# Kernel tuning notes

Hardware: AMD Instinct MI355X
Metric: run time of the kernel (lower is better)

## Reference

```python
import jax, jax.numpy as jnp
import numpy as np

S, D, E = 8192, 128, 48  # seq_len, embedding_dim, num pos tags (experts)

def setup_inputs() -> dict:
    key = jax.random.key(0)
    ks = jax.random.split(key, 8)
    sc = 1.0 / np.sqrt(D)
    return {
        "embs": jax.random.normal(ks[0], (S, D), dtype=jnp.float32),
        "pos_ids": jax.random.randint(ks[1], (S,), 0, E),
        "W_exp": jax.random.normal(ks[2], (E, D, D), dtype=jnp.float32) * sc,
        "b_exp": jax.random.normal(ks[3], (E, D), dtype=jnp.float32) * sc,
        "W_ih": jax.random.normal(ks[4], (4 * D, D), dtype=jnp.float32) * sc,
        "W_hh": jax.random.normal(ks[5], (4 * D, D), dtype=jnp.float32) * sc,
        "b_ih": jax.random.normal(ks[6], (4 * D,), dtype=jnp.float32) * sc,
        "b_hh": jax.random.normal(ks[7], (4 * D,), dtype=jnp.float32) * sc,
    }

def reference(embs, pos_ids, W_exp, b_exp, W_ih, W_hh, b_ih, b_hh):
    d = embs.shape[1]
    # --- per-token expert Linear (pos-tag-routed) ---
    # gather expert weights per token: [S, D, D], then per-token GEMV
    Wg = W_exp[pos_ids]                      # [S, D, D]
    bg = b_exp[pos_ids]                      # [S, D]
    z = jnp.einsum('sij,sj->si', Wg, embs) + bg  # [S, D]
    # --- 1-layer LSTM (PyTorch gate order: i, f, g, o) ---
    x_gates = z @ W_ih.T + b_ih + b_hh       # [S, 4D], precompute input contribution
    def step(carry, xg):
        h, c = carry
        gates = xg + h @ W_hh.T              # [4D]
        i, f, g, o = jnp.split(gates, 4)
        i = jax.nn.sigmoid(i)
        f = jax.nn.sigmoid(f)
        g = jnp.tanh(g)
        o = jax.nn.sigmoid(o)
        c = f * c + i * g
        h = o * jnp.tanh(c)
        return (h, c), h
    h0 = jnp.zeros((d,), dtype=embs.dtype)
    c0 = jnp.zeros((d,), dtype=embs.dtype)
    _, hs = jax.lax.scan(step, (h0, c0), x_gates)  # hs: [S, D]
    # --- max-pool over time; batch dim of 1 as in the torch module ---
    out = jnp.max(hs, axis=0)[None, :]       # [1, D]
    return out
```

## Files before the change

kernel.cpp:

```cpp
#include <hip/hip_runtime.h>
#include <math.h>


#define SEQ   8192
#define DIM   128
#define NGATE 512
#define NEXP  48

typedef _Float16 v8h  __attribute__((ext_vector_type(8)));
typedef float    v4f  __attribute__((ext_vector_type(4)));

__device__ __forceinline__ float sigm_fast(float x) {
    return __fdividef(1.0f, 1.0f + __expf(-x));
}
__device__ __forceinline__ float tanh_fast(float x) {
    float e = __expf(2.0f * x);
    return 1.0f - __fdividef(2.0f, e + 1.0f);
}
__device__ __forceinline__ v8h pack8(float4 a, float4 b) {
    v8h r;
    r[0]=(_Float16)a.x; r[1]=(_Float16)a.y; r[2]=(_Float16)a.z; r[3]=(_Float16)a.w;
    r[4]=(_Float16)b.x; r[5]=(_Float16)b.y; r[6]=(_Float16)b.z; r[7]=(_Float16)b.w;
    return r;
}
__device__ __forceinline__ float selv(v4f A, v4f B, int c) {
    float a01 = (c & 1) ? A[1] : A[0];
    float a23 = (c & 1) ? A[3] : A[2];
    float av  = (c & 2) ? a23 : a01;
    float b01 = (c & 1) ? B[1] : B[0];
    float b23 = (c & 1) ? B[3] : B[2];
    float bv  = (c & 2) ? b23 : b01;
    return (c & 4) ? bv : av;
}

__global__ __launch_bounds__(64) void expert_gemv(
    const float* __restrict__ embs, const int* __restrict__ pos_ids,
    const float* __restrict__ W_exp, const float* __restrict__ b_exp,
    float* __restrict__ xg)
{
    __shared__ float Wl[DIM * DIM];
    const int e     = blockIdx.x % NEXP;
    const int slice = blockIdx.x / NEXP;
    const int tid   = threadIdx.x;

    const float4* Wg = (const float4*)(W_exp + (size_t)e * DIM * DIM);
    #pragma unroll 4
    for (int it = 0; it < 64; ++it) {
        int idx = it * 64 + tid;
        int r = idx >> 5, c4 = idx & 31;
        float4 v = Wg[idx];
        *(float4*)&Wl[r * DIM + (((c4 ^ (r & 31))) << 2)] = v;
    }
    const float b0 = b_exp[e * DIM + tid];
    const float b1 = b_exp[e * DIM + 64 + tid];
    __syncthreads();

    const int r0 = tid, r1 = tid + 64;
    const int sw0 = r0 & 31, sw1 = r1 & 31;
    const int sBeg = slice * 1024, sEnd = sBeg + 1024;
    for (int base = sBeg; base < sEnd; base += 64) {
        int pid = pos_ids[base + tid];
        unsigned long long m = __ballot(pid == e);
        while (m) {
            int t = __builtin_ctzll(m);
            m &= m - 1;
            int s = base + t;
            const float4* ev = (const float4*)(embs + (size_t)s * DIM);
            float a0 = b0, a1 = b1;
            #pragma unroll
            for (int j4 = 0; j4 < 32; ++j4) {
                float4 x  = ev[j4];
                float4 w0 = *(const float4*)&Wl[r0 * DIM + ((j4 ^ sw0) << 2)];
                float4 w1 = *(const float4*)&Wl[r1 * DIM + ((j4 ^ sw1) << 2)];
                a0 = fmaf(w0.x,x.x,fmaf(w0.y,x.y,fmaf(w0.z,x.z,fmaf(w0.w,x.w,a0))));
                a1 = fmaf(w1.x,x.x,fmaf(w1.y,x.y,fmaf(w1.z,x.z,fmaf(w1.w,x.w,a1))));
            }
            float* zp = xg + (size_t)s * NGATE;
            zp[tid]      = a0;
            zp[tid + 64] = a1;
        }
    }
}

__global__ __launch_bounds__(256) void gate_gemm(
    const float* __restrict__ W_ih, const float* __restrict__ b_ih,
    const float* __restrict__ b_hh, float* __restrict__ xg)
{
    __shared__ float zl[32 * DIM];
    __shared__ float Wl[64 * DIM];
    const int tid = threadIdx.x;
    const int s0  = blockIdx.x * 32;

    #pragma unroll
    for (int it = 0; it < 4; ++it) {
        int idx = it * 256 + tid;
        int tok = idx >> 5, c4 = idx & 31;
        float4 v = *(const float4*)(xg + ((size_t)(s0 + tok)) * NGATE + (c4 << 2));
        *(float4*)&zl[tok * DIM + (((c4 ^ (tok & 31))) << 2)] = v;
    }
    __syncthreads();

    const int lane = tid & 63;
    const int tg   = tid >> 6;
    const int swr  = lane & 31;

    for (int ch = 0; ch < 8; ++ch) {
        #pragma unroll
        for (int it = 0; it < 8; ++it) {
            int idx = it * 256 + tid;
            int r = idx >> 5, c4 = idx & 31;
            float4 v = *(const float4*)(W_ih + ((size_t)(ch * 64 + r)) * DIM + (c4 << 2));
            *(float4*)&Wl[r * DIM + ((c4 ^ (r & 31)) << 2)] = v;
        }
        __syncthreads();

        const int row = ch * 64 + lane;
        const float bias = b_ih[row] + b_hh[row];
        float acc[8];
        #pragma unroll
        for (int k = 0; k < 8; ++k) acc[k] = bias;
        #pragma unroll 8
        for (int j4 = 0; j4 < 32; ++j4) {
            float4 w = *(const float4*)&Wl[lane * DIM + ((j4 ^ swr) << 2)];
            #pragma unroll
            for (int k = 0; k < 8; ++k) {
                int tok = tg * 8 + k;
                float4 z = *(const float4*)&zl[tok * DIM + ((j4 ^ (tok & 31)) << 2)];
                acc[k] = fmaf(w.x,z.x,fmaf(w.y,z.y,fmaf(w.z,z.z,fmaf(w.w,z.w,acc[k]))));
            }
        }
        const int pidx = ((row & 127) << 2) + (row >> 7);
        #pragma unroll
        for (int k = 0; k < 8; ++k) {
            int tok = tg * 8 + k;
            xg[((size_t)(s0 + tok)) * NGATE + pidx] = acc[k];
        }
        __syncthreads();
    }
}

__global__ __launch_bounds__(256, 1) void lstm_scan(
    const float* __restrict__ xg, const float* __restrict__ W_hh,
    float* __restrict__ out)
{
    const int T    = threadIdx.x;
    const int wg   = T >> 6;
    const int lane = T & 63;
    const int q    = lane >> 4;
    const int c    = lane & 15;
    const int q8   = q * 8;
    const int d    = wg * 32 + q * 4 + (c & 3) + ((c & 4) ? 16 : 0);
    const int dw   = d + ((c & 8) ? 128 : 0);

    __shared__ __align__(16) _Float16 hbuf[2][256];

    const int j0 = wg & 3, j1 = (wg + 1) & 3, j2 = (wg + 2) & 3, j3 = (wg + 3) & 3;
    const int bo0 = j0 * 32 + q8, bo1 = j1 * 32 + q8,
              bo2 = j2 * 32 + q8, bo3 = j3 * 32 + q8;

#define LOADA(G,H) \
    v8h a##G##H##0, a##G##H##1, a##G##H##2, a##G##H##3; { \
        const float4* p = (const float4*)(W_hh + \
            (size_t)((G) * 128 + wg * 32 + (H) * 16 + c) * DIM) + q * 2; \
        a##G##H##0 = pack8(p[8*j0], p[8*j0+1]); \
        a##G##H##1 = pack8(p[8*j1], p[8*j1+1]); \
        a##G##H##2 = pack8(p[8*j2], p[8*j2+1]); \
        a##G##H##3 = pack8(p[8*j3], p[8*j3+1]); }
    LOADA(0,0) LOADA(0,1) LOADA(1,0) LOADA(1,1)
    LOADA(2,0) LOADA(2,1) LOADA(3,0) LOADA(3,1)
#undef LOADA

    float cst  = 0.0f;
    float hmax = -INFINITY;

    if (T < DIM) hbuf[0][T] = (_Float16)0.0f;
    __syncthreads();

    v8h B0cur = *(const v8h*)&hbuf[0][bo0];

    const float* xp = xg + 4 * d;

    v4f X0, X1, X2, X3, X4, X5, X6, X7;
#define PRELD(n) { const float* _p = xp + (size_t)(n) * NGATE; \
    asm volatile("global_load_dwordx4 %0, %1, off" : "=v"(X##n) : "v"(_p)); }
    PRELD(0) PRELD(1) PRELD(2) PRELD(3) PRELD(4) PRELD(5) PRELD(6) PRELD(7)
#undef PRELD

    const v4f Z4 = {0.0f, 0.0f, 0.0f, 0.0f};

#define MF(G,H,K,B,CIN) __builtin_amdgcn_mfma_f32_16x16x32_f16(a##G##H##K, B, CIN, 0, 0, 0)

#define STEP(XV, tn, bf, nbf) { \
     \
    const v8h B1 = *(const v8h*)&hbuf[bf][bo1]; \
    const v8h B2 = *(const v8h*)&hbuf[bf][bo2]; \
    const v8h B3 = *(const v8h*)&hbuf[bf][bo3]; \
     \
    v4f c00 = MF(0,0,0,B0cur,Z4);  v4f c01 = MF(0,1,0,B0cur,Z4); \
    v4f c10 = MF(1,0,0,B0cur,Z4);  v4f c11 = MF(1,1,0,B0cur,Z4); \
    v4f c20 = MF(2,0,0,B0cur,Z4);  v4f c21 = MF(2,1,0,B0cur,Z4); \
    v4f c30 = MF(3,0,0,B0cur,Z4);  v4f c31 = MF(3,1,0,B0cur,Z4); \
    c00 = MF(0,0,1,B1,c00);  c01 = MF(0,1,1,B1,c01); \
    c10 = MF(1,0,1,B1,c10);  c11 = MF(1,1,1,B1,c11); \
    c20 = MF(2,0,1,B1,c20);  c21 = MF(2,1,1,B1,c21); \
    c30 = MF(3,0,1,B1,c30);  c31 = MF(3,1,1,B1,c31); \
    c00 = MF(0,0,2,B2,c00);  c01 = MF(0,1,2,B2,c01); \
    c10 = MF(1,0,2,B2,c10);  c11 = MF(1,1,2,B2,c11); \
    c20 = MF(2,0,2,B2,c20);  c21 = MF(2,1,2,B2,c21); \
    c30 = MF(3,0,2,B2,c30);  c31 = MF(3,1,2,B2,c31); \
    c00 = MF(0,0,3,B3,c00);  c01 = MF(0,1,3,B3,c01); \
    c10 = MF(1,0,3,B3,c10);  c11 = MF(1,1,3,B3,c11); \
    c20 = MF(2,0,3,B3,c20);  c21 = MF(2,1,3,B3,c21); \
    c30 = MF(3,0,3,B3,c30);  c31 = MF(3,1,3,B3,c31); \
     \
    asm volatile("s_waitcnt vmcnt(7)" : "+v"(XV));   \
    const v4f xcur = XV; \
    { const float* _p = xp + (size_t)(tn) * NGATE; \
      asm volatile("global_load_dwordx4 %0, %1, off" : "=v"(XV) : "v"(_p)); } \
     \
    const float pi = selv(c00, c01, c) + xcur[0]; \
    const float pf = selv(c10, c11, c) + xcur[1]; \
    const float pg = selv(c20, c21, c) + xcur[2]; \
    const float po = selv(c30, c31, c) + xcur[3]; \
    const float iv = sigm_fast(pi); \
    const float fv = sigm_fast(pf); \
    const float gv = tanh_fast(pg); \
    const float ov = sigm_fast(po); \
    cst = fmaf(fv, cst, iv * gv); \
    const float h = ov * tanh_fast(cst); \
    hmax = fmaxf(hmax, h); \
    hbuf[nbf][dw] = (_Float16)h; \
     \
     \
    B0cur = *(const v8h*)&hbuf[nbf][bo0]; \
    asm volatile("s_waitcnt lgkmcnt(0)\n\ts_barrier" ::: "memory"); }

    for (int t = 0; t < SEQ; t += 8) {
        const int tn0 = (t +  8 < SEQ) ? t +  8 : SEQ - 1;
        const int tn1 = (t +  9 < SEQ) ? t +  9 : SEQ - 1;
        const int tn2 = (t + 10 < SEQ) ? t + 10 : SEQ - 1;
        const int tn3 = (t + 11 < SEQ) ? t + 11 : SEQ - 1;
        const int tn4 = (t + 12 < SEQ) ? t + 12 : SEQ - 1;
        const int tn5 = (t + 13 < SEQ) ? t + 13 : SEQ - 1;
        const int tn6 = (t + 14 < SEQ) ? t + 14 : SEQ - 1;
        const int tn7 = (t + 15 < SEQ) ? t + 15 : SEQ - 1;
        STEP(X0, tn0, 0, 1)
        STEP(X1, tn1, 1, 0)
        STEP(X2, tn2, 0, 1)
        STEP(X3, tn3, 1, 0)
        STEP(X4, tn4, 0, 1)
        STEP(X5, tn5, 1, 0)
        STEP(X6, tn6, 0, 1)
        STEP(X7, tn7, 1, 0)
    }
#undef STEP
#undef MF

    if (c < 8) out[d] = hmax;
}

extern "C" void kernel_launch(void* const* d_in, const int* in_sizes, int n_in,
                              void* d_out, int out_size, void* d_ws, size_t ws_size,
                              hipStream_t stream)
{
    const float* embs  = (const float*)d_in[0];
    const int*   pos   = (const int*)  d_in[1];
    const float* W_exp = (const float*)d_in[2];
    const float* b_exp = (const float*)d_in[3];
    const float* W_ih  = (const float*)d_in[4];
    const float* W_hh  = (const float*)d_in[5];
    const float* b_ih  = (const float*)d_in[6];
    const float* b_hh  = (const float*)d_in[7];
    float* out = (float*)d_out;
    float* xg  = (float*)d_ws;

    expert_gemv<<<dim3(NEXP * 8), 64, 0, stream>>>(embs, pos, W_exp, b_exp, xg);
    gate_gemm  <<<dim3(256), 256, 0, stream>>>(W_ih, b_ih, b_hh, xg);
    lstm_scan  <<<dim3(1), 256, 0, stream>>>(xg, W_hh, out);
}
```

Baseline: 4.774 ms.

## Split LSTM recurrent gates between MFMA and VALU fdot2 paths

The input and cell gates (i, g) of the recurrent h·W_hh product move from MFMA to per-lane packed fp16 dot2 VALU instructions. Each lane keeps its own W_hh rows in registers and combines two k-halves with a ds_swizzle, while f and o stay on MFMA. This halves the serial MFMA chain per timestep so matrix and vector units can work in parallel. The cost is more VGPRs for the weights, extra LDS reads of h per step, and VALU work that could lengthen the critical path.

```diff
diff --git a/kernel.cpp b/kernel.cpp
--- a/kernel.cpp
+++ b/kernel.cpp
@@ -8,6 +8,7 @@
 #define NEXP  48
 
 typedef _Float16 v8h  __attribute__((ext_vector_type(8)));
+typedef _Float16 v2h  __attribute__((ext_vector_type(2)));
 typedef float    v4f  __attribute__((ext_vector_type(4)));
 
 __device__ __forceinline__ float sigm_fast(float x) {
@@ -32,6 +33,14 @@
     float bv  = (c & 2) ? b23 : b01;
     return (c & 4) ? bv : av;
 }
+__device__ __forceinline__ v2h pairof(v8h v, int p) {
+    v2h r; r[0] = v[2*p]; r[1] = v[2*p+1]; return r;
+}
+#if __has_builtin(__builtin_amdgcn_fdot2)
+#define DOT2(a,b,c) __builtin_amdgcn_fdot2((a),(b),(c),false)
+#else
+#define DOT2(a,b,c) ((c) + (float)(a)[0]*(float)(b)[0] + (float)(a)[1]*(float)(b)[1])
+#endif
 
 __global__ __launch_bounds__(64) void expert_gemv(
     const float* __restrict__ embs, const int* __restrict__ pos_ids,
@@ -149,8 +158,9 @@
     const int q    = lane >> 4;
     const int c    = lane & 15;
     const int q8   = q * 8;
-    const int d    = wg * 32 + q * 4 + (c & 3) + ((c & 4) ? 16 : 0);
-    const int dw   = d + ((c & 8) ? 128 : 0);
+    const int d     = wg * 32 + q * 4 + (c & 3) + ((c & 4) ? 16 : 0);
+    const int dw    = d + ((c & 8) ? 128 : 0);
+    const int khalf = (c & 8) ? 64 : 0;
 
     __shared__ __align__(16) _Float16 hbuf[2][256];
 
@@ -166,9 +176,20 @@
         a##G##H##1 = pack8(p[8*j1], p[8*j1+1]); \
         a##G##H##2 = pack8(p[8*j2], p[8*j2+1]); \
         a##G##H##3 = pack8(p[8*j3], p[8*j3+1]); }
-    LOADA(0,0) LOADA(0,1) LOADA(1,0) LOADA(1,1)
-    LOADA(2,0) LOADA(2,1) LOADA(3,0) LOADA(3,1)
+    LOADA(1,0) LOADA(1,1) LOADA(3,0) LOADA(3,1)
 #undef LOADA
+
+#define LOADW(P, G) \
+    v8h P##0,P##1,P##2,P##3,P##4,P##5,P##6,P##7; { \
+        const float4* p = (const float4*)(W_hh + \
+            (size_t)((G) * 128 + d) * DIM + khalf); \
+        P##0 = pack8(p[ 0], p[ 1]);  P##1 = pack8(p[ 2], p[ 3]); \
+        P##2 = pack8(p[ 4], p[ 5]);  P##3 = pack8(p[ 6], p[ 7]); \
+        P##4 = pack8(p[ 8], p[ 9]);  P##5 = pack8(p[10], p[11]); \
+        P##6 = pack8(p[12], p[13]);  P##7 = pack8(p[14], p[15]); }
+    LOADW(wi, 0)
+    LOADW(wq, 2)
+#undef LOADW
 
     float cst  = 0.0f;
     float hmax = -INFINITY;
@@ -190,47 +211,69 @@
 
 #define MF(G,H,K,B,CIN) __builtin_amdgcn_mfma_f32_16x16x32_f16(a##G##H##K, B, CIN, 0, 0, 0)
 
+#define DOTM(HM, WIM, WQM) { \
+    ai0 = DOT2(pairof(HM,0), pairof(WIM,0), ai0); \
+    ai1 = DOT2(pairof(HM,1), pairof(WIM,1), ai1); \
+    ai2 = DOT2(pairof(HM,2), pairof(WIM,2), ai2); \
+    ai3 = DOT2(pairof(HM,3), pairof(WIM,3), ai3); \
+    aq0 = DOT2(pairof(HM,0), pairof(WQM,0), aq0); \
+    aq1 = DOT2(pairof(HM,1), pairof(WQM,1), aq1); \
+    aq2 = DOT2(pairof(HM,2), pairof(WQM,2), aq2); \
+    aq3 = DOT2(pairof(HM,3), pairof(WQM,3), aq3); }
+
 #define STEP(XV, tn, bf, nbf) { \
      \
     const v8h B1 = *(const v8h*)&hbuf[bf][bo1]; \
     const v8h B2 = *(const v8h*)&hbuf[bf][bo2]; \
     const v8h B3 = *(const v8h*)&hbuf[bf][bo3]; \
      \
-    v4f c00 = MF(0,0,0,B0cur,Z4);  v4f c01 = MF(0,1,0,B0cur,Z4); \
     v4f c10 = MF(1,0,0,B0cur,Z4);  v4f c11 = MF(1,1,0,B0cur,Z4); \
-    v4f c20 = MF(2,0,0,B0cur,Z4);  v4f c21 = MF(2,1,0,B0cur,Z4); \
     v4f c30 = MF(3,0,0,B0cur,Z4);  v4f c31 = MF(3,1,0,B0cur,Z4); \
-    c00 = MF(0,0,1,B1,c00);  c01 = MF(0,1,1,B1,c01); \
+     \
+    const v8h h0 = *(const v8h*)&hbuf[bf][khalf +  0]; \
+    const v8h h1 = *(const v8h*)&hbuf[bf][khalf +  8]; \
+    const v8h h2 = *(const v8h*)&hbuf[bf][khalf + 16]; \
+    const v8h h3 = *(const v8h*)&hbuf[bf][khalf + 24]; \
+    const v8h h4 = *(const v8h*)&hbuf[bf][khalf + 32]; \
+    const v8h h5 = *(const v8h*)&hbuf[bf][khalf + 40]; \
+    const v8h h6 = *(const v8h*)&hbuf[bf][khalf + 48]; \
+    const v8h h7 = *(const v8h*)&hbuf[bf][khalf + 56]; \
+    float ai0=0.f, ai1=0.f, ai2=0.f, ai3=0.f; \
+    float aq0=0.f, aq1=0.f, aq2=0.f, aq3=0.f; \
+    DOTM(h0, wi0, wq0)  DOTM(h1, wi1, wq1) \
     c10 = MF(1,0,1,B1,c10);  c11 = MF(1,1,1,B1,c11); \
-    c20 = MF(2,0,1,B1,c20);  c21 = MF(2,1,1,B1,c21); \
     c30 = MF(3,0,1,B1,c30);  c31 = MF(3,1,1,B1,c31); \
-    c00 = MF(0,0,2,B2,c00);  c01 = MF(0,1,2,B2,c01); \
+    DOTM(h2, wi2, wq2)  DOTM(h3, wi3, wq3) \
     c10 = MF(1,0,2,B2,c10);  c11 = MF(1,1,2,B2,c11); \
-    c20 = MF(2,0,2,B2,c20);  c21 = MF(2,1,2,B2,c21); \
     c30 = MF(3,0,2,B2,c30);  c31 = MF(3,1,2,B2,c31); \
-    c00 = MF(0,0,3,B3,c00);  c01 = MF(0,1,3,B3,c01); \
+    DOTM(h4, wi4, wq4)  DOTM(h5, wi5, wq5) \
     c10 = MF(1,0,3,B3,c10);  c11 = MF(1,1,3,B3,c11); \
-    c20 = MF(2,0,3,B3,c20);  c21 = MF(2,1,3,B3,c21); \
     c30 = MF(3,0,3,B3,c30);  c31 = MF(3,1,3,B3,c31); \
+    DOTM(h6, wi6, wq6)  DOTM(h7, wi7, wq7) \
      \
     asm volatile("s_waitcnt vmcnt(7)" : "+v"(XV));   \
     const v4f xcur = XV; \
     { const float* _p = xp + (size_t)(tn) * NGATE; \
       asm volatile("global_load_dwordx4 %0, %1, off" : "=v"(XV) : "v"(_p)); } \
      \
-    const float pi = selv(c00, c01, c) + xcur[0]; \
+    float si = (ai0 + ai1) + (ai2 + ai3); \
+    float sq = (aq0 + aq1) + (aq2 + aq3); \
+    si += __int_as_float(__builtin_amdgcn_ds_swizzle(__float_as_int(si), 0x201F)); \
+    sq += __int_as_float(__builtin_amdgcn_ds_swizzle(__float_as_int(sq), 0x201F)); \
+    const float pi = si + xcur[0]; \
+    const float pg = sq + xcur[2]; \
+    const float iv = sigm_fast(pi); \
+    const float gv = tanh_fast(pg); \
+    const float ig = iv * gv; \
+     \
     const float pf = selv(c10, c11, c) + xcur[1]; \
-    const float pg = selv(c20, c21, c) + xcur[2]; \
     const float po = selv(c30, c31, c) + xcur[3]; \
-    const float iv = sigm_fast(pi); \
     const float fv = sigm_fast(pf); \
-    const float gv = tanh_fast(pg); \
     const float ov = sigm_fast(po); \
-    cst = fmaf(fv, cst, iv * gv); \
+    cst = fmaf(fv, cst, ig); \
     const float h = ov * tanh_fast(cst); \
     hmax = fmaxf(hmax, h); \
     hbuf[nbf][dw] = (_Float16)h; \
-     \
      \
     B0cur = *(const v8h*)&hbuf[nbf][bo0]; \
     asm volatile("s_waitcnt lgkmcnt(0)\n\ts_barrier" ::: "memory"); }
@@ -254,6 +297,7 @@
         STEP(X7, tn7, 1, 0)
     }
 #undef STEP
+#undef DOTM
 #undef MF
 
     if (c < 8) out[d] = hmax;
```

After: 5.212 ms. 9.2% more time.

## Split LSTM scan across eight wavefronts to halve per-wave MFMA chain

Applied to the files above, without the earlier changes.

The recurrent scan kernel now launches 512 threads (8 waves) instead of 256. Each wave owns 16 hidden rows per gate and issues 16 MFMAs per timestep instead of 32. This shortens the serial matrix work on the per-step critical path of the latency-bound recurrence, at the cost of a barrier across twice as many waves each step. The hand-written inline-asm prefetch with explicit waitcnt is replaced by plain vector loads, so load/wait scheduling is left to the compiler.

```diff
diff --git a/kernel.cpp b/kernel.cpp
--- a/kernel.cpp
+++ b/kernel.cpp
@@ -23,14 +23,10 @@
     r[4]=(_Float16)b.x; r[5]=(_Float16)b.y; r[6]=(_Float16)b.z; r[7]=(_Float16)b.w;
     return r;
 }
-__device__ __forceinline__ float selv(v4f A, v4f B, int c) {
-    float a01 = (c & 1) ? A[1] : A[0];
-    float a23 = (c & 1) ? A[3] : A[2];
-    float av  = (c & 2) ? a23 : a01;
-    float b01 = (c & 1) ? B[1] : B[0];
-    float b23 = (c & 1) ? B[3] : B[2];
-    float bv  = (c & 2) ? b23 : b01;
-    return (c & 4) ? bv : av;
+__device__ __forceinline__ float sel4(v4f V, int c) {
+    float v01 = (c & 1) ? V[1] : V[0];
+    float v23 = (c & 1) ? V[3] : V[2];
+    return (c & 2) ? v23 : v01;
 }
 
 __global__ __launch_bounds__(64) void expert_gemv(
@@ -139,35 +135,31 @@
     }
 }
 
-__global__ __launch_bounds__(256, 1) void lstm_scan(
+__global__ __launch_bounds__(512, 2) void lstm_scan(
     const float* __restrict__ xg, const float* __restrict__ W_hh,
     float* __restrict__ out)
 {
     const int T    = threadIdx.x;
-    const int wg   = T >> 6;
+    const int w8   = T >> 6;
     const int lane = T & 63;
     const int q    = lane >> 4;
     const int c    = lane & 15;
     const int q8   = q * 8;
-    const int d    = wg * 32 + q * 4 + (c & 3) + ((c & 4) ? 16 : 0);
-    const int dw   = d + ((c & 8) ? 128 : 0);
-
-    __shared__ __align__(16) _Float16 hbuf[2][256];
-
-    const int j0 = wg & 3, j1 = (wg + 1) & 3, j2 = (wg + 2) & 3, j3 = (wg + 3) & 3;
-    const int bo0 = j0 * 32 + q8, bo1 = j1 * 32 + q8,
-              bo2 = j2 * 32 + q8, bo3 = j3 * 32 + q8;
-
-#define LOADA(G,H) \
-    v8h a##G##H##0, a##G##H##1, a##G##H##2, a##G##H##3; { \
+    const int m    = c >> 2;
+    const int d    = w8 * 16 + q * 4 + (c & 3);
+    const int dw   = d + 128 * m;
+
+    __shared__ __align__(16) _Float16 hbuf[2][512];
+
+#define LOADA(G) \
+    v8h a##G##_0, a##G##_1, a##G##_2, a##G##_3; { \
         const float4* p = (const float4*)(W_hh + \
-            (size_t)((G) * 128 + wg * 32 + (H) * 16 + c) * DIM) + q * 2; \
-        a##G##H##0 = pack8(p[8*j0], p[8*j0+1]); \
-        a##G##H##1 = pack8(p[8*j1], p[8*j1+1]); \
-        a##G##H##2 = pack8(p[8*j2], p[8*j2+1]); \
-        a##G##H##3 = pack8(p[8*j3], p[8*j3+1]); }
-    LOADA(0,0) LOADA(0,1) LOADA(1,0) LOADA(1,1)
-    LOADA(2,0) LOADA(2,1) LOADA(3,0) LOADA(3,1)
+            (size_t)((G) * 128 + w8 * 16 + c) * DIM) + q * 2; \
+        a##G##_0 = pack8(p[ 0], p[ 1]); \
+        a##G##_1 = pack8(p[ 8], p[ 9]); \
+        a##G##_2 = pack8(p[16], p[17]); \
+        a##G##_3 = pack8(p[24], p[25]); }
+    LOADA(0) LOADA(1) LOADA(2) LOADA(3)
 #undef LOADA
 
     float cst  = 0.0f;
@@ -176,52 +168,39 @@
     if (T < DIM) hbuf[0][T] = (_Float16)0.0f;
     __syncthreads();
 
-    v8h B0cur = *(const v8h*)&hbuf[0][bo0];
-
     const float* xp = xg + 4 * d;
 
     v4f X0, X1, X2, X3, X4, X5, X6, X7;
-#define PRELD(n) { const float* _p = xp + (size_t)(n) * NGATE; \
-    asm volatile("global_load_dwordx4 %0, %1, off" : "=v"(X##n) : "v"(_p)); }
+#define PRELD(n) X##n = *(const v4f*)(xp + (size_t)(n) * NGATE);
     PRELD(0) PRELD(1) PRELD(2) PRELD(3) PRELD(4) PRELD(5) PRELD(6) PRELD(7)
 #undef PRELD
 
     const v4f Z4 = {0.0f, 0.0f, 0.0f, 0.0f};
 
-#define MF(G,H,K,B,CIN) __builtin_amdgcn_mfma_f32_16x16x32_f16(a##G##H##K, B, CIN, 0, 0, 0)
+#define MF(G,K,B,CIN) __builtin_amdgcn_mfma_f32_16x16x32_f16(a##G##_##K, B, CIN, 0, 0, 0)
 
 #define STEP(XV, tn, bf, nbf) { \
+    const v8h B0 = *(const v8h*)&hbuf[bf][ 0 + q8]; \
+    const v8h B1 = *(const v8h*)&hbuf[bf][32 + q8]; \
+    const v8h B2 = *(const v8h*)&hbuf[bf][64 + q8]; \
+    const v8h B3 = *(const v8h*)&hbuf[bf][96 + q8]; \
      \
-    const v8h B1 = *(const v8h*)&hbuf[bf][bo1]; \
-    const v8h B2 = *(const v8h*)&hbuf[bf][bo2]; \
-    const v8h B3 = *(const v8h*)&hbuf[bf][bo3]; \
+    v4f ci = MF(0,0,B0,Z4);  v4f cf = MF(1,0,B0,Z4); \
+    v4f cg = MF(2,0,B0,Z4);  v4f co = MF(3,0,B0,Z4); \
      \
-    v4f c00 = MF(0,0,0,B0cur,Z4);  v4f c01 = MF(0,1,0,B0cur,Z4); \
-    v4f c10 = MF(1,0,0,B0cur,Z4);  v4f c11 = MF(1,1,0,B0cur,Z4); \
-    v4f c20 = MF(2,0,0,B0cur,Z4);  v4f c21 = MF(2,1,0,B0cur,Z4); \
-    v4f c30 = MF(3,0,0,B0cur,Z4);  v4f c31 = MF(3,1,0,B0cur,Z4); \
-    c00 = MF(0,0,1,B1,c00);  c01 = MF(0,1,1,B1,c01); \
-    c10 = MF(1,0,1,B1,c10);  c11 = MF(1,1,1,B1,c11); \
-    c20 = MF(2,0,1,B1,c20);  c21 = MF(2,1,1,B1,c21); \
-    c30 = MF(3,0,1,B1,c30);  c31 = MF(3,1,1,B1,c31); \
-    c00 = MF(0,0,2,B2,c00);  c01 = MF(0,1,2,B2,c01); \
-    c10 = MF(1,0,2,B2,c10);  c11 = MF(1,1,2,B2,c11); \
-    c20 = MF(2,0,2,B2,c20);  c21 = MF(2,1,2,B2,c21); \
-    c30 = MF(3,0,2,B2,c30);  c31 = MF(3,1,2,B2,c31); \
-    c00 = MF(0,0,3,B3,c00);  c01 = MF(0,1,3,B3,c01); \
-    c10 = MF(1,0,3,B3,c10);  c11 = MF(1,1,3,B3,c11); \
-    c20 = MF(2,0,3,B3,c20);  c21 = MF(2,1,3,B3,c21); \
-    c30 = MF(3,0,3,B3,c30);  c31 = MF(3,1,3,B3,c31); \
+    const v4f xcur = XV; \
+    XV = *(const v4f*)(xp + (size_t)(tn) * NGATE); \
+    ci = MF(0,1,B1,ci);  cf = MF(1,1,B1,cf); \
+    cg = MF(2,1,B1,cg);  co = MF(3,1,B1,co); \
+    ci = MF(0,2,B2,ci);  cf = MF(1,2,B2,cf); \
+    cg = MF(2,2,B2,cg);  co = MF(3,2,B2,co); \
+    ci = MF(0,3,B3,ci);  cf = MF(1,3,B3,cf); \
+    cg = MF(2,3,B3,cg);  co = MF(3,3,B3,co); \
      \
-    asm volatile("s_waitcnt vmcnt(7)" : "+v"(XV));   \
-    const v4f xcur = XV; \
-    { const float* _p = xp + (size_t)(tn) * NGATE; \
-      asm volatile("global_load_dwordx4 %0, %1, off" : "=v"(XV) : "v"(_p)); } \
-     \
-    const float pi = selv(c00, c01, c) + xcur[0]; \
-    const float pf = selv(c10, c11, c) + xcur[1]; \
-    const float pg = selv(c20, c21, c) + xcur[2]; \
-    const float po = selv(c30, c31, c) + xcur[3]; \
+    const float pi = sel4(ci, c) + xcur[0]; \
+    const float pf = sel4(cf, c) + xcur[1]; \
+    const float pg = sel4(cg, c) + xcur[2]; \
+    const float po = sel4(co, c) + xcur[3]; \
     const float iv = sigm_fast(pi); \
     const float fv = sigm_fast(pf); \
     const float gv = tanh_fast(pg); \
@@ -230,9 +209,6 @@
     const float h = ov * tanh_fast(cst); \
     hmax = fmaxf(hmax, h); \
     hbuf[nbf][dw] = (_Float16)h; \
-     \
-     \
-    B0cur = *(const v8h*)&hbuf[nbf][bo0]; \
     asm volatile("s_waitcnt lgkmcnt(0)\n\ts_barrier" ::: "memory"); }
 
     for (int t = 0; t < SEQ; t += 8) {
@@ -256,7 +232,7 @@
 #undef STEP
 #undef MF
 
-    if (c < 8) out[d] = hmax;
+    if (c < 4) out[d] = hmax;
 }
 
 extern "C" void kernel_launch(void* const* d_in, const int* in_sizes, int n_in,
@@ -276,5 +252,5 @@
 
     expert_gemv<<<dim3(NEXP * 8), 64, 0, stream>>>(embs, pos, W_exp, b_exp, xg);
     gate_gemm  <<<dim3(256), 256, 0, stream>>>(W_ih, b_ih, b_hh, xg);
-    lstm_scan  <<<dim3(1), 256, 0, stream>>>(xg, W_hh, out);
-}
+    lstm_scan  <<<dim3(1), 512, 0, stream>>>(xg, W_hh, out);
+}
```

Measured after the change: 5.057 ms. +5.9%, slower.
